# Performance work log

Hardware: AMD Instinct MI355X
Metric: run time of the kernel (lower is better)

## Reference

```python
import jax, jax.numpy as jnp
import numpy as np

FP8_MAX = 448.0  # float8_e4m3fn max


def _quant_fp8(x, scale):
    # static scaled fp8 quant: clamp to fp8 range, round via dtype cast
    q = jnp.clip(x / scale, -FP8_MAX, FP8_MAX).astype(jnp.float8_e4m3fn)
    return q.astype(jnp.float32)


def setup_inputs() -> dict:
    key = jax.random.key(0)
    ks = jax.random.split(key, 6)
    T, H = 8192, 4096
    I = 2 * H
    hidden_states = jax.random.normal(ks[0], (T, H), dtype=jnp.float32)
    residual = jax.random.normal(ks[1], (T, H), dtype=jnp.float32)
    norm_weight = jax.random.uniform(ks[2], (H,), dtype=jnp.float32)
    # fp8 weight: torch stores rand().to(fp8); emulate by rounding through fp8
    w_raw = jax.random.uniform(ks[3], (H, I), dtype=jnp.float32)  # already transposed [H, I]
    w = w_raw.astype(jnp.float8_e4m3fn).astype(jnp.float32)
    scale = jax.random.uniform(ks[4], (1,), dtype=jnp.float32) + 0.01
    wscale = jax.random.uniform(ks[5], (1,), dtype=jnp.float32) + 0.01
    return {"hidden_states": hidden_states, "residual": residual,
            "norm_weight": norm_weight, "w": w, "scale": scale, "wscale": wscale}


def reference(hidden_states, residual, norm_weight, w, scale, wscale):
    eps = 1e-6
    H = norm_weight.shape[0]
    x = hidden_states.reshape(-1, H)
    # tensor_model_parallel_all_reduce on a single device = identity
    all_reduce = x
    # fused add + RMSNorm (vllm RMSNorm with residual): residual_out = x + residual
    residual_out = all_reduce + residual
    var = jnp.mean(residual_out * residual_out, axis=-1, keepdims=True)
    norm_out = residual_out * jax.lax.rsqrt(var + eps) * norm_weight
    # static fp8 quant of activations, fp8 GEMM, dequant by scale*wscale
    q = _quant_fp8(norm_out, scale)  # [T, H]
    out = jnp.matmul(q, w) * (scale * wscale)  # [T, I]
    return (out, residual_out)
```

## Files before the change

kernel.cpp:

```cpp
#include <hip/hip_runtime.h>
#include <stdint.h>


typedef float float16v __attribute__((ext_vector_type(16)));
typedef int   int8v    __attribute__((ext_vector_type(8)));

#define GLOAD_LDS16(gp, lp)                                                    \
    __builtin_amdgcn_global_load_lds(                                          \
        (const __attribute__((address_space(1))) void*)(gp),                   \
        (__attribute__((address_space(3))) void*)(lp), 16, 0, 0)

#define MFMA_SCALE1(a, b, c)                                                   \
    __builtin_amdgcn_mfma_scale_f32_32x32x64_f8f6f4(                           \
        (a), (b), (c), 0, 0, 0, 0x7f7f7f7f, 0, 0x7f7f7f7f)

__global__ void __launch_bounds__(256) wconv_kernel(
    const float* __restrict__ w, uint8_t* __restrict__ wt, int K, int N) {
    __shared__ uint8_t tile[64 * 64];
    const int k0 = blockIdx.y * 64;
    const int n0 = blockIdx.x * 64;
    const int t = threadIdx.x;
    const int c4 = t & 15;
    const int r = t >> 4;

#pragma unroll
    for (int p = 0; p < 4; ++p) {
        const int k = r + p * 16;
        const float4 v = *(const float4*)(w + (size_t)(k0 + k) * N + n0 + c4 * 4);
        const int pk0 = __builtin_amdgcn_cvt_pk_fp8_f32(v.x, v.y, 0, false);
        const int pk1 = __builtin_amdgcn_cvt_pk_fp8_f32(v.z, v.w, 0, false);
        tile[(c4 * 4 + 0) * 64 + k] = (uint8_t)(pk0 & 0xff);
        tile[(c4 * 4 + 1) * 64 + k] = (uint8_t)((pk0 >> 8) & 0xff);
        tile[(c4 * 4 + 2) * 64 + k] = (uint8_t)(pk1 & 0xff);
        tile[(c4 * 4 + 3) * 64 + k] = (uint8_t)((pk1 >> 8) & 0xff);
    }
    __syncthreads();
    const int n_local = t >> 2;
    const int ch = t & 3;
    const uint4 val = *(const uint4*)(&tile[n_local * 64 + ch * 16]);
    const int n = n0 + n_local;
    const size_t tile_idx = (size_t)(n >> 7) * (K >> 6) + (k0 >> 6);
    const int c = ((n >> 5) & 3) * 4 + ch;
    *(uint4*)(wt + tile_idx * 8192 + c * 512 + (n & 31) * 16) = val;
}

__global__ void __launch_bounds__(256) norm_quant_kernel(
    const float* __restrict__ hs, const float* __restrict__ res,
    const float* __restrict__ nw, const float* __restrict__ scale,
    float* __restrict__ resid_out, uint8_t* __restrict__ q, int H) {
    __shared__ float sm[4096];
    __shared__ float wsum[4];
    __shared__ float s_inv;
    const int row = blockIdx.x;
    const int t = threadIdx.x;
    const float* hrow = hs + (size_t)row * H;
    const float* rrow = res + (size_t)row * H;
    float* orow = resid_out + (size_t)row * H;

    float acc = 0.f;
#pragma unroll
    for (int p = 0; p < 4; ++p) {
        const int c = p * 1024 + t * 4;
        const float4 h = *(const float4*)(hrow + c);
        const float4 r = *(const float4*)(rrow + c);
        float4 s;
        s.x = h.x + r.x; s.y = h.y + r.y; s.z = h.z + r.z; s.w = h.w + r.w;
        *(float4*)(orow + c) = s;
        *(float4*)(&sm[c]) = s;
        acc += s.x * s.x + s.y * s.y + s.z * s.z + s.w * s.w;
    }
#pragma unroll
    for (int off = 32; off; off >>= 1) acc += __shfl_down(acc, off);
    if ((t & 63) == 0) wsum[t >> 6] = acc;
    __syncthreads();
    if (t == 0) {
        const float tot = wsum[0] + wsum[1] + wsum[2] + wsum[3];
        s_inv = 1.0f / sqrtf(tot / (float)H + 1e-6f);
    }
    __syncthreads();
    const float inv = s_inv;
    const float sval = scale[0];

    const int k0 = t * 16;
    uint32_t words[4];
#pragma unroll
    for (int i = 0; i < 4; ++i) {
        const float4 s = *(const float4*)(&sm[k0 + i * 4]);
        const float4 wv = *(const float4*)(nw + k0 + i * 4);
        float q0 = (s.x * inv * wv.x) / sval;
        float q1 = (s.y * inv * wv.y) / sval;
        float q2 = (s.z * inv * wv.z) / sval;
        float q3 = (s.w * inv * wv.w) / sval;
        q0 = fminf(fmaxf(q0, -448.f), 448.f);
        q1 = fminf(fmaxf(q1, -448.f), 448.f);
        q2 = fminf(fmaxf(q2, -448.f), 448.f);
        q3 = fminf(fmaxf(q3, -448.f), 448.f);
        int pk = __builtin_amdgcn_cvt_pk_fp8_f32(q0, q1, 0, false);
        pk = __builtin_amdgcn_cvt_pk_fp8_f32(q2, q3, pk, true);
        words[i] = (uint32_t)pk;
    }
    const int kt = t >> 2;
    const int ch = t & 3;
    const size_t tile_idx = (size_t)(row >> 7) * (H >> 6) + kt;
    const int c = ((row >> 5) & 3) * 4 + ch;
    uint4 val;
    val.x = words[0]; val.y = words[1]; val.z = words[2]; val.w = words[3];
    *(uint4*)(q + tile_idx * 8192 + c * 512 + (row & 31) * 16) = val;
}

static __device__ __forceinline__ int8v ldfrag(const uint8_t* p) {
    const uint4 lo = *(const uint4*)p;
    const uint4 hi = *(const uint4*)(p + 512);
    int8v r = {(int)lo.x, (int)lo.y, (int)lo.z, (int)lo.w,
               (int)hi.x, (int)hi.y, (int)hi.z, (int)hi.w};
    return r;
}

__global__ void __launch_bounds__(512, 2) gemm_fp8_kernel(
    const uint8_t* __restrict__ A,
    const uint8_t* __restrict__ B,
    float* __restrict__ C,
    const float* __restrict__ scale, const float* __restrict__ wscale,
    int M, int N, int K) {
    __shared__ uint8_t lds[3 * 32768];

    const int t = threadIdx.x;
    const int wid = t >> 6;
    const int lane = t & 63;
    const int wr = wid >> 2;
    const int wc = wid & 3;

    const int id = blockIdx.x;
    const int wg = (id & 7) * ((int)gridDim.x >> 3) + (id >> 3);
    const int nbn = N >> 8;
    const int bm = wg / nbn;
    const int bn = wg % nbn;

    const int nkt = K >> 6;
    const uint8_t* a0s = A + (size_t)(2 * bm) * nkt * 8192;
    const uint8_t* a1s = a0s + (size_t)nkt * 8192;
    const uint8_t* b0s = B + (size_t)(2 * bn) * nkt * 8192;
    const uint8_t* b1s = b0s + (size_t)nkt * 8192;
    const int o16 = t * 16;

#pragma unroll
    for (int u = 0; u < 2; ++u) {
        uint8_t* dst = lds + u * 32768;
        const size_t ofs = (size_t)u * 8192 + o16;
        GLOAD_LDS16(a0s + ofs, dst + o16);
        GLOAD_LDS16(a1s + ofs, dst + 8192 + o16);
        GLOAD_LDS16(b0s + ofs, dst + 16384 + o16);
        GLOAD_LDS16(b1s + ofs, dst + 24576 + o16);
    }

    const int lgrp = (lane >> 5) * 1024;
    const int lrow = (lane & 31) * 16;
    int aoff[4], boff[2];
#pragma unroll
    for (int mb = 0; mb < 4; ++mb) {
        const int r32 = wr * 4 + mb;
        aoff[mb] = (r32 >> 2) * 8192 + (r32 & 3) * 2048 + lgrp + lrow;
    }
#pragma unroll
    for (int nb = 0; nb < 2; ++nb) {
        const int c32 = wc * 2 + nb;
        boff[nb] = 16384 + (c32 >> 2) * 8192 + (c32 & 3) * 2048 + lgrp + lrow;
    }

    float16v acc[4][2] = {};

    int cur = 0, pfs = 2;
    for (int kt = 0; kt < nkt; ++kt) {
        asm volatile("s_waitcnt vmcnt(4)" ::: "memory");
        __builtin_amdgcn_s_barrier();

        const uint8_t* sl = lds + cur * 32768;
        uint8_t* pdst = lds + pfs * 32768;
        const int pf = (kt + 2 < nkt) ? (kt + 2) : (nkt - 1);
        const size_t pofs = (size_t)pf * 8192 + o16;

        const int8v b0 = ldfrag(sl + boff[0]);
        const int8v b1 = ldfrag(sl + boff[1]);
        const int8v a0 = ldfrag(sl + aoff[0]);
        const int8v a1 = ldfrag(sl + aoff[1]);
        GLOAD_LDS16(a0s + pofs, pdst + o16);
        GLOAD_LDS16(a1s + pofs, pdst + 8192 + o16);
        __builtin_amdgcn_sched_barrier(0);
        __builtin_amdgcn_s_setprio(1);
        acc[0][0] = MFMA_SCALE1(a0, b0, acc[0][0]);
        acc[0][1] = MFMA_SCALE1(a0, b1, acc[0][1]);
        acc[1][0] = MFMA_SCALE1(a1, b0, acc[1][0]);
        acc[1][1] = MFMA_SCALE1(a1, b1, acc[1][1]);
        __builtin_amdgcn_s_setprio(0);

        const int8v a2 = ldfrag(sl + aoff[2]);
        const int8v a3 = ldfrag(sl + aoff[3]);
        GLOAD_LDS16(b0s + pofs, pdst + 16384 + o16);
        GLOAD_LDS16(b1s + pofs, pdst + 24576 + o16);
        __builtin_amdgcn_sched_barrier(0);
        __builtin_amdgcn_s_setprio(1);
        acc[2][0] = MFMA_SCALE1(a2, b0, acc[2][0]);
        acc[2][1] = MFMA_SCALE1(a2, b1, acc[2][1]);
        acc[3][0] = MFMA_SCALE1(a3, b0, acc[3][0]);
        acc[3][1] = MFMA_SCALE1(a3, b1, acc[3][1]);
        __builtin_amdgcn_s_setprio(0);

        cur = (cur == 2) ? 0 : cur + 1;
        pfs = (pfs == 2) ? 0 : pfs + 1;
    }

    const float f = scale[0] * wscale[0];
    const int col = lane & 31;
    const int rb4 = (lane >> 5) * 4;
#pragma unroll
    for (int mb = 0; mb < 4; ++mb) {
#pragma unroll
        for (int nb = 0; nb < 2; ++nb) {
#pragma unroll
            for (int reg = 0; reg < 16; ++reg) {
                const int r = (reg & 3) + 8 * (reg >> 2) + rb4;
                const size_t gr = (size_t)(bm * 256 + wr * 128 + mb * 32 + r);
                const size_t gc = (size_t)(bn * 256 + wc * 64 + nb * 32 + col);
                C[gr * N + gc] = acc[mb][nb][reg] * f;
            }
        }
    }
}

extern "C" void kernel_launch(void* const* d_in, const int* in_sizes, int n_in,
                              void* d_out, int out_size, void* d_ws, size_t ws_size,
                              hipStream_t stream) {
    const float* hs     = (const float*)d_in[0];
    const float* res    = (const float*)d_in[1];
    const float* nw     = (const float*)d_in[2];
    const float* w      = (const float*)d_in[3];
    const float* scale  = (const float*)d_in[4];
    const float* wscale = (const float*)d_in[5];

    const int H = in_sizes[2];
    const int T = in_sizes[0] / H;
    const int I = in_sizes[3] / H;

    float* out       = (float*)d_out;
    float* resid_out = out + (size_t)T * I;
    uint8_t* q  = (uint8_t*)d_ws;
    uint8_t* wt = q + (size_t)T * H;

    wconv_kernel<<<dim3(I / 64, H / 64), 256, 0, stream>>>(w, wt, H, I);
    norm_quant_kernel<<<T, 256, 0, stream>>>(hs, res, nw, scale, resid_out, q, H);
    gemm_fp8_kernel<<<(T / 256) * (I / 256), 512, 0, stream>>>(
        q, wt, out, scale, wscale, T, I, H);
}
```

Measured before the change: 465.0 us.

## Restructure fp8 GEMM main loop into double-buffered two-tile phases with per-MFMA barriers

Replaces the triple-buffered single-k-tile loop with a double buffer that holds two k-tiles per stage, using 128KB of LDS. Each k-tile is split into four phases. Every phase loads one A fragment, issues one global-to-LDS prefetch, hits a workgroup barrier, then runs two MFMAs. The goal is to interleave prefetch, LDS reads and MFMAs more finely and keep the waves in lockstep. The cost is many more barriers per tile and an lgkmcnt(0) wait before each MFMA pair. The loop also assumes the k-tile count is even.

```diff
diff --git a/kernel.cpp b/kernel.cpp
--- a/kernel.cpp
+++ b/kernel.cpp
@@ -122,7 +122,7 @@
     float* __restrict__ C,
     const float* __restrict__ scale, const float* __restrict__ wscale,
     int M, int N, int K) {
-    __shared__ uint8_t lds[3 * 32768];
+    __shared__ uint8_t lds[2 * 65536];
 
     const int t = threadIdx.x;
     const int wid = t >> 6;
@@ -137,77 +137,115 @@
     const int bn = wg % nbn;
 
     const int nkt = K >> 6;
+    const int niter = nkt >> 1;
     const uint8_t* a0s = A + (size_t)(2 * bm) * nkt * 8192;
     const uint8_t* a1s = a0s + (size_t)nkt * 8192;
     const uint8_t* b0s = B + (size_t)(2 * bn) * nkt * 8192;
     const uint8_t* b1s = b0s + (size_t)nkt * 8192;
     const int o16 = t * 16;
 
-#pragma unroll
-    for (int u = 0; u < 2; ++u) {
-        uint8_t* dst = lds + u * 32768;
-        const size_t ofs = (size_t)u * 8192 + o16;
-        GLOAD_LDS16(a0s + ofs, dst + o16);
-        GLOAD_LDS16(a1s + ofs, dst + 8192 + o16);
-        GLOAD_LDS16(b0s + ofs, dst + 16384 + o16);
-        GLOAD_LDS16(b1s + ofs, dst + 24576 + o16);
-    }
-
     const int lgrp = (lane >> 5) * 1024;
     const int lrow = (lane & 31) * 16;
-    int aoff[4], boff[2];
-#pragma unroll
-    for (int mb = 0; mb < 4; ++mb) {
-        const int r32 = wr * 4 + mb;
-        aoff[mb] = (r32 >> 2) * 8192 + (r32 & 3) * 2048 + lgrp + lrow;
-    }
-#pragma unroll
-    for (int nb = 0; nb < 2; ++nb) {
-        const int c32 = wc * 2 + nb;
-        boff[nb] = 16384 + (c32 >> 2) * 8192 + (c32 & 3) * 2048 + lgrp + lrow;
-    }
+    const int r32b = wr * 4;
+    const int aoff0 = ((r32b + 0) >> 2) * 8192 + ((r32b + 0) & 3) * 2048 + lgrp + lrow;
+    const int aoff1 = ((r32b + 1) >> 2) * 8192 + ((r32b + 1) & 3) * 2048 + lgrp + lrow;
+    const int aoff2 = ((r32b + 2) >> 2) * 8192 + ((r32b + 2) & 3) * 2048 + lgrp + lrow;
+    const int aoff3 = ((r32b + 3) >> 2) * 8192 + ((r32b + 3) & 3) * 2048 + lgrp + lrow;
+    const int c32b = wc * 2;
+    const int boff0 = 16384 + ((c32b + 0) >> 2) * 8192 + ((c32b + 0) & 3) * 2048 + lgrp + lrow;
+    const int boff1 = 16384 + ((c32b + 1) >> 2) * 8192 + ((c32b + 1) & 3) * 2048 + lgrp + lrow;
 
     float16v acc[4][2] = {};
 
-    int cur = 0, pfs = 2;
-    for (int kt = 0; kt < nkt; ++kt) {
+    GLOAD_LDS16(a0s + o16, lds + o16);
+    GLOAD_LDS16(a1s + o16, lds + 8192 + o16);
+    GLOAD_LDS16(b0s + o16, lds + 16384 + o16);
+    GLOAD_LDS16(b1s + o16, lds + 24576 + o16);
+    GLOAD_LDS16(a0s + 8192 + o16, lds + 32768 + o16);
+    GLOAD_LDS16(a1s + 8192 + o16, lds + 40960 + o16);
+    GLOAD_LDS16(b0s + 8192 + o16, lds + 49152 + o16);
+    GLOAD_LDS16(b1s + 8192 + o16, lds + 57344 + o16);
+
+    int8v bfr0, bfr1;
+
+#define PH_MFMA(AFR, MB)                                                       \
+    asm volatile("s_waitcnt lgkmcnt(0)" ::: "memory");                         \
+    __builtin_amdgcn_sched_barrier(0);                                         \
+    __builtin_amdgcn_s_setprio(1);                                             \
+    acc[MB][0] = MFMA_SCALE1(AFR, bfr0, acc[MB][0]);                           \
+    acc[MB][1] = MFMA_SCALE1(AFR, bfr1, acc[MB][1]);                           \
+    __builtin_amdgcn_s_setprio(0);                                             \
+    __builtin_amdgcn_s_barrier();
+
+    int buf = 0;
+    for (int i = 0; i < niter; ++i) {
+        const uint8_t* sl0 = lds + buf * 65536;
+        const uint8_t* sl1 = sl0 + 32768;
+        uint8_t* ob = lds + (buf ^ 1) * 65536;
+        const int nt0 = (2 * i + 2 < nkt) ? (2 * i + 2) : (nkt - 1);
+        const int nt1 = (2 * i + 3 < nkt) ? (2 * i + 3) : (nkt - 1);
+        const size_t s0 = (size_t)nt0 * 8192 + o16;
+        const size_t s1 = (size_t)nt1 * 8192 + o16;
+
         asm volatile("s_waitcnt vmcnt(4)" ::: "memory");
+        GLOAD_LDS16(a0s + s0, ob + o16);
         __builtin_amdgcn_s_barrier();
-
-        const uint8_t* sl = lds + cur * 32768;
-        uint8_t* pdst = lds + pfs * 32768;
-        const int pf = (kt + 2 < nkt) ? (kt + 2) : (nkt - 1);
-        const size_t pofs = (size_t)pf * 8192 + o16;
-
-        const int8v b0 = ldfrag(sl + boff[0]);
-        const int8v b1 = ldfrag(sl + boff[1]);
-        const int8v a0 = ldfrag(sl + aoff[0]);
-        const int8v a1 = ldfrag(sl + aoff[1]);
-        GLOAD_LDS16(a0s + pofs, pdst + o16);
-        GLOAD_LDS16(a1s + pofs, pdst + 8192 + o16);
         __builtin_amdgcn_sched_barrier(0);
-        __builtin_amdgcn_s_setprio(1);
-        acc[0][0] = MFMA_SCALE1(a0, b0, acc[0][0]);
-        acc[0][1] = MFMA_SCALE1(a0, b1, acc[0][1]);
-        acc[1][0] = MFMA_SCALE1(a1, b0, acc[1][0]);
-        acc[1][1] = MFMA_SCALE1(a1, b1, acc[1][1]);
-        __builtin_amdgcn_s_setprio(0);
-
-        const int8v a2 = ldfrag(sl + aoff[2]);
-        const int8v a3 = ldfrag(sl + aoff[3]);
-        GLOAD_LDS16(b0s + pofs, pdst + 16384 + o16);
-        GLOAD_LDS16(b1s + pofs, pdst + 24576 + o16);
+        bfr0 = ldfrag(sl0 + boff0);
+        bfr1 = ldfrag(sl0 + boff1);
+        {
+            const int8v af = ldfrag(sl0 + aoff0);
+            PH_MFMA(af, 0)
+        }
+        {
+            const int8v af = ldfrag(sl0 + aoff1);
+            GLOAD_LDS16(a1s + s0, ob + 8192 + o16);
+            __builtin_amdgcn_s_barrier();
+            PH_MFMA(af, 1)
+        }
+        {
+            const int8v af = ldfrag(sl0 + aoff2);
+            GLOAD_LDS16(b0s + s0, ob + 16384 + o16);
+            __builtin_amdgcn_s_barrier();
+            PH_MFMA(af, 2)
+        }
+        {
+            const int8v af = ldfrag(sl0 + aoff3);
+            GLOAD_LDS16(b1s + s0, ob + 24576 + o16);
+            __builtin_amdgcn_s_barrier();
+            PH_MFMA(af, 3)
+        }
+        asm volatile("s_waitcnt vmcnt(4)" ::: "memory");
+        GLOAD_LDS16(a0s + s1, ob + 32768 + o16);
+        __builtin_amdgcn_s_barrier();
         __builtin_amdgcn_sched_barrier(0);
-        __builtin_amdgcn_s_setprio(1);
-        acc[2][0] = MFMA_SCALE1(a2, b0, acc[2][0]);
-        acc[2][1] = MFMA_SCALE1(a2, b1, acc[2][1]);
-        acc[3][0] = MFMA_SCALE1(a3, b0, acc[3][0]);
-        acc[3][1] = MFMA_SCALE1(a3, b1, acc[3][1]);
-        __builtin_amdgcn_s_setprio(0);
-
-        cur = (cur == 2) ? 0 : cur + 1;
-        pfs = (pfs == 2) ? 0 : pfs + 1;
-    }
+        bfr0 = ldfrag(sl1 + boff0);
+        bfr1 = ldfrag(sl1 + boff1);
+        {
+            const int8v af = ldfrag(sl1 + aoff0);
+            PH_MFMA(af, 0)
+        }
+        {
+            const int8v af = ldfrag(sl1 + aoff1);
+            GLOAD_LDS16(a1s + s1, ob + 40960 + o16);
+            __builtin_amdgcn_s_barrier();
+            PH_MFMA(af, 1)
+        }
+        {
+            const int8v af = ldfrag(sl1 + aoff2);
+            GLOAD_LDS16(b0s + s1, ob + 49152 + o16);
+            __builtin_amdgcn_s_barrier();
+            PH_MFMA(af, 2)
+        }
+        {
+            const int8v af = ldfrag(sl1 + aoff3);
+            GLOAD_LDS16(b1s + s1, ob + 57344 + o16);
+            __builtin_amdgcn_s_barrier();
+            PH_MFMA(af, 3)
+        }
+        buf ^= 1;
+    }
+#undef PH_MFMA
 
     const float f = scale[0] * wscale[0];
     const int col = lane & 31;
```

New measurement: 623.4 us. +34.1%, slower.

## Use 4-wave workgroups with 128x128 per-wave tiles in fp8 GEMM

Applied to the files above, without the earlier changes.

The GEMM workgroup drops from 8 waves to 4 waves. Each wave now computes a 128x128 sub-tile with 4x4 MFMA accumulators instead of 128x64, which raises fragment reuse per LDS read. Each thread issues twice as many global-to-LDS loads per stage, and the wait count rises to match. The interleaved scheduling barriers and priority hints are removed. The cost is higher register pressure, with 256 accumulator floats per lane, lower occupancy, and less explicit overlap of loads and MFMA.

```diff
diff --git a/kernel.cpp b/kernel.cpp
--- a/kernel.cpp
+++ b/kernel.cpp
@@ -116,7 +116,7 @@
     return r;
 }
 
-__global__ void __launch_bounds__(512, 2) gemm_fp8_kernel(
+__global__ void __launch_bounds__(256, 1) gemm_fp8_kernel(
     const uint8_t* __restrict__ A,
     const uint8_t* __restrict__ B,
     float* __restrict__ C,
@@ -127,8 +127,8 @@
     const int t = threadIdx.x;
     const int wid = t >> 6;
     const int lane = t & 63;
-    const int wr = wid >> 2;
-    const int wc = wid & 3;
+    const int wr = wid >> 1;
+    const int wc = wid & 1;
 
     const int id = blockIdx.x;
     const int wg = (id & 7) * ((int)gridDim.x >> 3) + (id >> 3);
@@ -143,67 +143,55 @@
     const uint8_t* b1s = b0s + (size_t)nkt * 8192;
     const int o16 = t * 16;
 
+    const int lgrp = (lane >> 5) * 1024;
+    const int lrow = (lane & 31) * 16;
+    const int abase = wr * 8192 + lgrp + lrow;
+    const int bbase = 16384 + wc * 8192 + lgrp + lrow;
+
+    float16v acc[4][4] = {};
+
 #pragma unroll
     for (int u = 0; u < 2; ++u) {
         uint8_t* dst = lds + u * 32768;
         const size_t ofs = (size_t)u * 8192 + o16;
-        GLOAD_LDS16(a0s + ofs, dst + o16);
-        GLOAD_LDS16(a1s + ofs, dst + 8192 + o16);
-        GLOAD_LDS16(b0s + ofs, dst + 16384 + o16);
-        GLOAD_LDS16(b1s + ofs, dst + 24576 + o16);
-    }
-
-    const int lgrp = (lane >> 5) * 1024;
-    const int lrow = (lane & 31) * 16;
-    int aoff[4], boff[2];
-#pragma unroll
-    for (int mb = 0; mb < 4; ++mb) {
-        const int r32 = wr * 4 + mb;
-        aoff[mb] = (r32 >> 2) * 8192 + (r32 & 3) * 2048 + lgrp + lrow;
-    }
-#pragma unroll
-    for (int nb = 0; nb < 2; ++nb) {
-        const int c32 = wc * 2 + nb;
-        boff[nb] = 16384 + (c32 >> 2) * 8192 + (c32 & 3) * 2048 + lgrp + lrow;
-    }
-
-    float16v acc[4][2] = {};
+        GLOAD_LDS16(a0s + ofs,        dst + o16);
+        GLOAD_LDS16(a0s + ofs + 4096, dst + 4096 + o16);
+        GLOAD_LDS16(a1s + ofs,        dst + 8192 + o16);
+        GLOAD_LDS16(a1s + ofs + 4096, dst + 12288 + o16);
+        GLOAD_LDS16(b0s + ofs,        dst + 16384 + o16);
+        GLOAD_LDS16(b0s + ofs + 4096, dst + 20480 + o16);
+        GLOAD_LDS16(b1s + ofs,        dst + 24576 + o16);
+        GLOAD_LDS16(b1s + ofs + 4096, dst + 28672 + o16);
+    }
 
     int cur = 0, pfs = 2;
     for (int kt = 0; kt < nkt; ++kt) {
-        asm volatile("s_waitcnt vmcnt(4)" ::: "memory");
+        asm volatile("s_waitcnt vmcnt(8)" ::: "memory");
         __builtin_amdgcn_s_barrier();
 
         const uint8_t* sl = lds + cur * 32768;
-        uint8_t* pdst = lds + pfs * 32768;
+        uint8_t* pd = lds + pfs * 32768;
         const int pf = (kt + 2 < nkt) ? (kt + 2) : (nkt - 1);
         const size_t pofs = (size_t)pf * 8192 + o16;
-
-        const int8v b0 = ldfrag(sl + boff[0]);
-        const int8v b1 = ldfrag(sl + boff[1]);
-        const int8v a0 = ldfrag(sl + aoff[0]);
-        const int8v a1 = ldfrag(sl + aoff[1]);
-        GLOAD_LDS16(a0s + pofs, pdst + o16);
-        GLOAD_LDS16(a1s + pofs, pdst + 8192 + o16);
-        __builtin_amdgcn_sched_barrier(0);
-        __builtin_amdgcn_s_setprio(1);
-        acc[0][0] = MFMA_SCALE1(a0, b0, acc[0][0]);
-        acc[0][1] = MFMA_SCALE1(a0, b1, acc[0][1]);
-        acc[1][0] = MFMA_SCALE1(a1, b0, acc[1][0]);
-        acc[1][1] = MFMA_SCALE1(a1, b1, acc[1][1]);
-        __builtin_amdgcn_s_setprio(0);
-
-        const int8v a2 = ldfrag(sl + aoff[2]);
-        const int8v a3 = ldfrag(sl + aoff[3]);
-        GLOAD_LDS16(b0s + pofs, pdst + 16384 + o16);
-        GLOAD_LDS16(b1s + pofs, pdst + 24576 + o16);
-        __builtin_amdgcn_sched_barrier(0);
-        __builtin_amdgcn_s_setprio(1);
-        acc[2][0] = MFMA_SCALE1(a2, b0, acc[2][0]);
-        acc[2][1] = MFMA_SCALE1(a2, b1, acc[2][1]);
-        acc[3][0] = MFMA_SCALE1(a3, b0, acc[3][0]);
-        acc[3][1] = MFMA_SCALE1(a3, b1, acc[3][1]);
-        __builtin_amdgcn_s_setprio(0);
+        GLOAD_LDS16(a0s + pofs,        pd + o16);
+        GLOAD_LDS16(a0s + pofs + 4096, pd + 4096 + o16);
+        GLOAD_LDS16(a1s + pofs,        pd + 8192 + o16);
+        GLOAD_LDS16(a1s + pofs + 4096, pd + 12288 + o16);
+        GLOAD_LDS16(b0s + pofs,        pd + 16384 + o16);
+        GLOAD_LDS16(b0s + pofs + 4096, pd + 20480 + o16);
+        GLOAD_LDS16(b1s + pofs,        pd + 24576 + o16);
+        GLOAD_LDS16(b1s + pofs + 4096, pd + 28672 + o16);
+
+        int8v a[4], b[4];
+#pragma unroll
+        for (int i = 0; i < 4; ++i) a[i] = ldfrag(sl + abase + i * 2048);
+#pragma unroll
+        for (int j = 0; j < 4; ++j) b[j] = ldfrag(sl + bbase + j * 2048);
+#pragma unroll
+        for (int i = 0; i < 4; ++i)
+#pragma unroll
+            for (int j = 0; j < 4; ++j)
+                acc[i][j] = MFMA_SCALE1(a[i], b[j], acc[i][j]);
 
         cur = (cur == 2) ? 0 : cur + 1;
         pfs = (pfs == 2) ? 0 : pfs + 1;
@@ -215,12 +203,12 @@
 #pragma unroll
     for (int mb = 0; mb < 4; ++mb) {
 #pragma unroll
-        for (int nb = 0; nb < 2; ++nb) {
+        for (int nb = 0; nb < 4; ++nb) {
 #pragma unroll
             for (int reg = 0; reg < 16; ++reg) {
                 const int r = (reg & 3) + 8 * (reg >> 2) + rb4;
                 const size_t gr = (size_t)(bm * 256 + wr * 128 + mb * 32 + r);
-                const size_t gc = (size_t)(bn * 256 + wc * 64 + nb * 32 + col);
+                const size_t gc = (size_t)(bn * 256 + wc * 128 + nb * 32 + col);
                 C[gr * N + gc] = acc[mb][nb][reg] * f;
             }
         }
@@ -248,6 +236,6 @@
 
     wconv_kernel<<<dim3(I / 64, H / 64), 256, 0, stream>>>(w, wt, H, I);
     norm_quant_kernel<<<T, 256, 0, stream>>>(hs, res, nw, scale, resid_out, q, H);
-    gemm_fp8_kernel<<<(T / 256) * (I / 256), 512, 0, stream>>>(
+    gemm_fp8_kernel<<<(T / 256) * (I / 256), 256, 0, stream>>>(
         q, wt, out, scale, wscale, T, I, H);
 }
```

Measured after the change: 559.3 us. 1.2x slower.

## Load B fragments directly from global into registers, stage only A through LDS

Applied to the files above, without the earlier changes.

Removes B from the LDS pipeline: each wave now loads its B fragments straight from global memory into registers one k-tile ahead, while A is still staged through a triple-buffered LDS ring, now half the size. The loop is unrolled by two to alternate B register sets and use compile-time buffer slots. This cuts LDS traffic and footprint and may allow higher occupancy, but B reads are no longer shared across the waves of a workgroup, so global and L2 traffic goes up. The vmcnt accounting changes too, with direct global loads and the LDS DMA loads now mixed under one counter.

```diff
diff --git a/kernel.cpp b/kernel.cpp
--- a/kernel.cpp
+++ b/kernel.cpp
@@ -122,7 +122,7 @@
     float* __restrict__ C,
     const float* __restrict__ scale, const float* __restrict__ wscale,
     int M, int N, int K) {
-    __shared__ uint8_t lds[3 * 32768];
+    __shared__ uint8_t lds[3 * 16384];
 
     const int t = threadIdx.x;
     const int wid = t >> 6;
@@ -143,71 +143,83 @@
     const uint8_t* b1s = b0s + (size_t)nkt * 8192;
     const int o16 = t * 16;
 
-#pragma unroll
-    for (int u = 0; u < 2; ++u) {
-        uint8_t* dst = lds + u * 32768;
-        const size_t ofs = (size_t)u * 8192 + o16;
-        GLOAD_LDS16(a0s + ofs, dst + o16);
-        GLOAD_LDS16(a1s + ofs, dst + 8192 + o16);
-        GLOAD_LDS16(b0s + ofs, dst + 16384 + o16);
-        GLOAD_LDS16(b1s + ofs, dst + 24576 + o16);
-    }
-
     const int lgrp = (lane >> 5) * 1024;
     const int lrow = (lane & 31) * 16;
-    int aoff[4], boff[2];
+
+    int aoff[4];
 #pragma unroll
     for (int mb = 0; mb < 4; ++mb) {
         const int r32 = wr * 4 + mb;
         aoff[mb] = (r32 >> 2) * 8192 + (r32 & 3) * 2048 + lgrp + lrow;
     }
+    const uint8_t* bsrc[2];
+    int bofs[2];
 #pragma unroll
     for (int nb = 0; nb < 2; ++nb) {
         const int c32 = wc * 2 + nb;
-        boff[nb] = 16384 + (c32 >> 2) * 8192 + (c32 & 3) * 2048 + lgrp + lrow;
+        bsrc[nb] = (c32 & 4) ? b1s : b0s;
+        bofs[nb] = (c32 & 3) * 2048 + lgrp + lrow;
     }
 
     float16v acc[4][2] = {};
 
-    int cur = 0, pfs = 2;
-    for (int kt = 0; kt < nkt; ++kt) {
-        asm volatile("s_waitcnt vmcnt(4)" ::: "memory");
+#define STAGE_A(u, slot)                                                       \
+    {                                                                          \
+        const size_t _o = (size_t)(u) * 8192 + o16;                            \
+        uint8_t* _d = lds + (slot) * 16384;                                    \
+        GLOAD_LDS16(a0s + _o, _d + o16);                                       \
+        GLOAD_LDS16(a1s + _o, _d + 8192 + o16);                                \
+    }
+
+#define LOAD_B(u, dst)                                                         \
+    {                                                                          \
+        const size_t _b = (size_t)(u) * 8192;                                  \
+        dst[0] = ldfrag(bsrc[0] + _b + bofs[0]);                               \
+        dst[1] = ldfrag(bsrc[1] + _b + bofs[1]);                               \
+    }
+
+#define DO_MFMA(slot, breg)                                                    \
+    {                                                                          \
+        const uint8_t* _s = lds + (slot) * 16384;                              \
+        int8v _a[4];                                                           \
+        _Pragma("unroll") for (int mb = 0; mb < 4; ++mb)                       \
+            _a[mb] = ldfrag(_s + aoff[mb]);                                    \
+        _Pragma("unroll") for (int mb = 0; mb < 4; ++mb) {                     \
+            acc[mb][0] = MFMA_SCALE1(_a[mb], breg[0], acc[mb][0]);             \
+            acc[mb][1] = MFMA_SCALE1(_a[mb], breg[1], acc[mb][1]);             \
+        }                                                                      \
+    }
+
+    int8v b_even[2], b_odd[2];
+
+    STAGE_A(0, 0)
+    STAGE_A(1, 1)
+    LOAD_B(0, b_even)
+
+    for (int kt = 0; kt < nkt; kt += 2) {
+        const int s0 = kt % 3, s1 = (kt + 1) % 3, s2 = (kt + 2) % 3;
+        asm volatile("s_waitcnt vmcnt(6)" ::: "memory");
         __builtin_amdgcn_s_barrier();
-
-        const uint8_t* sl = lds + cur * 32768;
-        uint8_t* pdst = lds + pfs * 32768;
-        const int pf = (kt + 2 < nkt) ? (kt + 2) : (nkt - 1);
-        const size_t pofs = (size_t)pf * 8192 + o16;
-
-        const int8v b0 = ldfrag(sl + boff[0]);
-        const int8v b1 = ldfrag(sl + boff[1]);
-        const int8v a0 = ldfrag(sl + aoff[0]);
-        const int8v a1 = ldfrag(sl + aoff[1]);
-        GLOAD_LDS16(a0s + pofs, pdst + o16);
-        GLOAD_LDS16(a1s + pofs, pdst + 8192 + o16);
-        __builtin_amdgcn_sched_barrier(0);
-        __builtin_amdgcn_s_setprio(1);
-        acc[0][0] = MFMA_SCALE1(a0, b0, acc[0][0]);
-        acc[0][1] = MFMA_SCALE1(a0, b1, acc[0][1]);
-        acc[1][0] = MFMA_SCALE1(a1, b0, acc[1][0]);
-        acc[1][1] = MFMA_SCALE1(a1, b1, acc[1][1]);
-        __builtin_amdgcn_s_setprio(0);
-
-        const int8v a2 = ldfrag(sl + aoff[2]);
-        const int8v a3 = ldfrag(sl + aoff[3]);
-        GLOAD_LDS16(b0s + pofs, pdst + 16384 + o16);
-        GLOAD_LDS16(b1s + pofs, pdst + 24576 + o16);
-        __builtin_amdgcn_sched_barrier(0);
-        __builtin_amdgcn_s_setprio(1);
-        acc[2][0] = MFMA_SCALE1(a2, b0, acc[2][0]);
-        acc[2][1] = MFMA_SCALE1(a2, b1, acc[2][1]);
-        acc[3][0] = MFMA_SCALE1(a3, b0, acc[3][0]);
-        acc[3][1] = MFMA_SCALE1(a3, b1, acc[3][1]);
-        __builtin_amdgcn_s_setprio(0);
-
-        cur = (cur == 2) ? 0 : cur + 1;
-        pfs = (pfs == 2) ? 0 : pfs + 1;
-    }
+        {
+            const int pf = (kt + 2 < nkt) ? (kt + 2) : (nkt - 1);
+            STAGE_A(pf, s2)
+            const int bu = (kt + 1 < nkt) ? (kt + 1) : (nkt - 1);
+            LOAD_B(bu, b_odd)
+            DO_MFMA(s0, b_even)
+        }
+        asm volatile("s_waitcnt vmcnt(6)" ::: "memory");
+        __builtin_amdgcn_s_barrier();
+        {
+            const int pf = (kt + 3 < nkt) ? (kt + 3) : (nkt - 1);
+            STAGE_A(pf, s0)
+            const int bu = (kt + 2 < nkt) ? (kt + 2) : (nkt - 1);
+            LOAD_B(bu, b_even)
+            DO_MFMA(s1, b_odd)
+        }
+    }
+#undef STAGE_A
+#undef LOAD_B
+#undef DO_MFMA
 
     const float f = scale[0] * wscale[0];
     const int col = lane & 31;
```

Result: slower. 505.7 us (+8.8%).
